# Optimization experiments

Hardware: AMD Instinct MI355X
Metric: run time of the kernel (lower is better)

The kernel has to match this reference:

```python
import jax, jax.numpy as jnp
import numpy as np

D_MODEL = 256
N_HEADS = 8
N_LEVELS = 3
N_POINTS = 4
HEAD_DIM = D_MODEL // N_HEADS
SPATIAL_SHAPES = [(80, 80), (40, 40), (20, 20)]
B = 16
LEN_Q = 300
N_TOTAL = sum(h * w for h, w in SPATIAL_SHAPES)  # 8400
N_LP = N_LEVELS * N_POINTS


def setup_inputs() -> dict:
    key = jax.random.key(0)
    ks = jax.random.split(key, 8)
    s = 0.02
    return {
        "query": jax.random.normal(ks[0], (B, LEN_Q, D_MODEL), jnp.float32),
        "reference_points": jax.random.uniform(ks[1], (B, LEN_Q, N_LEVELS, 2), jnp.float32),
        "input_flatten": jax.random.normal(ks[2], (B, N_TOTAL, D_MODEL), jnp.float32),
        "W_off": jax.random.normal(ks[3], (D_MODEL, N_HEADS * N_LP * 2), jnp.float32) * s,
        "b_off": jnp.zeros((N_HEADS * N_LP * 2,), jnp.float32),
        "W_attn": jax.random.normal(ks[4], (D_MODEL, N_HEADS * N_LP), jnp.float32) * s,
        "b_attn": jnp.zeros((N_HEADS * N_LP,), jnp.float32),
        "W_val": jax.random.normal(ks[5], (D_MODEL, D_MODEL), jnp.float32) * s,
        "b_val": jnp.zeros((D_MODEL,), jnp.float32),
        "W_out": jax.random.normal(ks[6], (D_MODEL, D_MODEL), jnp.float32) * s,
        "b_out": jnp.zeros((D_MODEL,), jnp.float32),
    }


def _ms_deform_core(value, sampling_locations, attention_weights):
    # value: (B, n_heads, head_dim, N_total); locations: (B, Lq, H, L, P, 2) in [0,1]
    Bq, Lq = sampling_locations.shape[0], sampling_locations.shape[1]
    BN = Bq * N_HEADS
    grids = 2.0 * sampling_locations - 1.0
    starts = np.cumsum([0] + [h * w for h, w in SPATIAL_SHAPES])
    sampled_levels = []
    for lid, (H, W) in enumerate(SPATIAL_SHAPES):
        val_l = value[..., starts[lid]:starts[lid + 1]]                    # (B,H,hd,HW)
        val_flat = val_l.reshape(BN, HEAD_DIM, H * W).transpose(0, 2, 1)   # (BN,HW,hd)
        g = grids[:, :, :, lid].transpose(0, 2, 1, 3, 4).reshape(BN, Lq, N_POINTS, 2)
        ix = ((g[..., 0] + 1.0) * W - 1.0) / 2.0
        iy = ((g[..., 1] + 1.0) * H - 1.0) / 2.0
        ix0 = jnp.floor(ix).astype(jnp.int32)
        iy0 = jnp.floor(iy).astype(jnp.int32)
        ix1 = ix0 + 1
        iy1 = iy0 + 1
        fx = (ix - ix0.astype(ix.dtype))[..., None]
        fy = (iy - iy0.astype(iy.dtype))[..., None]

        def corner(iyc, ixc):
            valid = ((ixc >= 0) & (ixc < W) & (iyc >= 0) & (iyc < H)).astype(val_flat.dtype)
            idx = (jnp.clip(iyc, 0, H - 1) * W + jnp.clip(ixc, 0, W - 1))
            idx = idx.reshape(BN, Lq * N_POINTS, 1)
            v = jnp.take_along_axis(val_flat, idx, axis=1)
            return v.reshape(BN, Lq, N_POINTS, HEAD_DIM) * valid[..., None]

        v00 = corner(iy0, ix0)
        v01 = corner(iy0, ix1)
        v10 = corner(iy1, ix0)
        v11 = corner(iy1, ix1)
        sampled = ((1 - fx) * (1 - fy)) * v00 + (fx * (1 - fy)) * v01 \
                + ((1 - fx) * fy) * v10 + (fx * fy) * v11
        sampled_levels.append(sampled.transpose(0, 3, 1, 2))               # (BN,hd,Lq,P)
    sv = jnp.stack(sampled_levels, axis=-2).reshape(BN, HEAD_DIM, Lq, N_LP)
    a = attention_weights.transpose(0, 2, 1, 3).reshape(BN, 1, Lq, N_LP)
    out = jnp.sum(sv * a, axis=-1)                                         # (BN,hd,Lq)
    return out.reshape(Bq, D_MODEL, Lq).transpose(0, 2, 1)                 # (B,Lq,D)


def reference(query, reference_points, input_flatten,
              W_off, b_off, W_attn, b_attn, W_val, b_val, W_out, b_out):
    Bq, Lq = query.shape[0], query.shape[1]
    value = input_flatten @ W_val + b_val
    value = value.reshape(Bq, -1, N_HEADS, HEAD_DIM).transpose(0, 2, 3, 1)  # (B,H,hd,N)
    off = (query @ W_off + b_off).reshape(Bq, Lq, N_HEADS, N_LEVELS, N_POINTS, 2)
    attn = jax.nn.softmax((query @ W_attn + b_attn).reshape(Bq, Lq, N_HEADS, N_LP), axis=-1)
    # offset normalizer is (W,H) per level (x first)
    norm = jnp.array([[w, h] for h, w in SPATIAL_SHAPES], jnp.float32)
    loc = reference_points[:, :, None, :, None, :] + off / norm[None, None, None, :, None, :]
    out = _ms_deform_core(value, loc, attn)
    return out @ W_out + b_out
```

## Files before the change

### kernel.cpp

```cpp
#include <hip/hip_runtime.h>
#include <hip/hip_bf16.h>

#define DM 256
#define NH 8
#define HD 32
#define NLV 3
#define NPT 4
#define NLP 12
#define BB 16
#define LQ 300
#define NT 8400
#define MROWS (BB * NT)
#define QROWS (BB * LQ)
#define KP 40

typedef __bf16 bf16x8 __attribute__((ext_vector_type(8)));
typedef float  f32x16 __attribute__((ext_vector_type(16)));

__global__ void k_wt(const float* __restrict__ W_val,
                     const float* __restrict__ W_off,
                     const float* __restrict__ W_attn,
                     __hip_bfloat16* __restrict__ Wt,
                     __hip_bfloat16* __restrict__ Wt2)
{
    const int n = blockIdx.x;
    const int k = threadIdx.x;
    if (n < 256) {
        Wt[(size_t)(k >> 5) * 8192 + n * 32 + (k & 31)] =
            __float2bfloat16(W_val[(size_t)k * 256 + n]);
    } else {
        const int n2 = n - 256;
        float v = (n2 < 192) ? W_off[(size_t)k * 192 + n2]
                             : W_attn[(size_t)k * 96 + (n2 - 192)];
        Wt2[(size_t)(k >> 5) * 9216 + n2 * 32 + (k & 31)] = __float2bfloat16(v);
    }
}

__global__ __launch_bounds__(256) void k_valproj(
    const float* __restrict__ A,
    const __hip_bfloat16* __restrict__ Wt,
    const float* __restrict__ bias,
    __hip_bfloat16* __restrict__ V)
{
    __shared__ __hip_bfloat16 As[64 * KP];
    __shared__ __hip_bfloat16 Ws[256 * KP];

    const int t    = threadIdx.x;
    const int m0   = blockIdx.x * 64;
    const int wave = t >> 6;
    const int lane = t & 63;
    const int lm   = lane & 31;
    const int lk   = (lane >> 5) * 8;

    f32x16 acc[2][2];
#pragma unroll
    for (int i = 0; i < 2; i++)
#pragma unroll
        for (int j = 0; j < 2; j++)
#pragma unroll
            for (int e = 0; e < 16; e++) acc[i][j][e] = 0.f;

    const int ar = t >> 2;
    const int ak = (t & 3) * 8;

    for (int kt = 0; kt < 256; kt += 32) {
        {
            const float* ap = A + (size_t)(m0 + ar) * 256 + kt + ak;
            float4 a0 = *(const float4*)ap;
            float4 a1 = *(const float4*)(ap + 4);
            union { __hip_bfloat162 h2[4]; bf16x8 v; } ua;
            ua.h2[0] = __float22bfloat162_rn(make_float2(a0.x, a0.y));
            ua.h2[1] = __float22bfloat162_rn(make_float2(a0.z, a0.w));
            ua.h2[2] = __float22bfloat162_rn(make_float2(a1.x, a1.y));
            ua.h2[3] = __float22bfloat162_rn(make_float2(a1.z, a1.w));
            *(bf16x8*)(As + ar * KP + ak) = ua.v;
        }
        {
            const __hip_bfloat16* wp = Wt + (size_t)(kt >> 5) * 8192 + t * 32;
            bf16x8 w0 = *(const bf16x8*)(wp + 0);
            bf16x8 w1 = *(const bf16x8*)(wp + 8);
            bf16x8 w2 = *(const bf16x8*)(wp + 16);
            bf16x8 w3 = *(const bf16x8*)(wp + 24);
            __hip_bfloat16* wd = Ws + t * KP;
            *(bf16x8*)(wd + 0)  = w0;
            *(bf16x8*)(wd + 8)  = w1;
            *(bf16x8*)(wd + 16) = w2;
            *(bf16x8*)(wd + 24) = w3;
        }
        __syncthreads();

#pragma unroll
        for (int kk = 0; kk < 32; kk += 16) {
            bf16x8 af0 = *(const bf16x8*)(As + (0 * 32 + lm) * KP + kk + lk);
            bf16x8 af1 = *(const bf16x8*)(As + (1 * 32 + lm) * KP + kk + lk);
            bf16x8 bf0 = *(const bf16x8*)(Ws + (wave * 64 + 0 * 32 + lm) * KP + kk + lk);
            bf16x8 bf1 = *(const bf16x8*)(Ws + (wave * 64 + 1 * 32 + lm) * KP + kk + lk);
            acc[0][0] = __builtin_amdgcn_mfma_f32_32x32x16_bf16(af0, bf0, acc[0][0], 0, 0, 0);
            acc[0][1] = __builtin_amdgcn_mfma_f32_32x32x16_bf16(af0, bf1, acc[0][1], 0, 0, 0);
            acc[1][0] = __builtin_amdgcn_mfma_f32_32x32x16_bf16(af1, bf0, acc[1][0], 0, 0, 0);
            acc[1][1] = __builtin_amdgcn_mfma_f32_32x32x16_bf16(af1, bf1, acc[1][1], 0, 0, 0);
        }
        __syncthreads();
    }

#pragma unroll
    for (int ni = 0; ni < 2; ni++) {
        const int n  = wave * 64 + ni * 32 + lm;
        const float bn = bias[n];
        const int h  = n >> 5;
        const int d  = n & 31;
#pragma unroll
        for (int mi = 0; mi < 2; mi++) {
#pragma unroll
            for (int r = 0; r < 16; r++) {
                int rl = (r & 3) + 8 * (r >> 2) + 4 * (lane >> 5);
                int m  = m0 + mi * 32 + rl;
                int b  = m / NT;
                int pos = m - b * NT;
                V[((size_t)(b * NH + h) * NT + pos) * HD + d] =
                    __float2bfloat16(acc[mi][ni][r] + bn);
            }
        }
    }
}

__global__ __launch_bounds__(192) void k_offattn(
    const float* __restrict__ Q,
    const __hip_bfloat16* __restrict__ Wt2,
    const float* __restrict__ boff,
    const float* __restrict__ battn,
    float* __restrict__ off_out,
    float* __restrict__ attn_out)
{
    __shared__ __hip_bfloat16 As[32 * KP];
    __shared__ __hip_bfloat16 Ws[288 * KP];

    const int t    = threadIdx.x;
    const int m0   = blockIdx.x * 32;
    const int wave = t >> 6;
    const int lane = t & 63;
    const int lm   = lane & 31;
    const int lk   = (lane >> 5) * 8;

    f32x16 acc[3];
#pragma unroll
    for (int j = 0; j < 3; j++)
#pragma unroll
        for (int e = 0; e < 16; e++) acc[j][e] = 0.f;

    for (int kt = 0; kt < 256; kt += 32) {
        if (t < 128) {
            const int ar = t >> 2;
            const int ak = (t & 3) * 8;
            const float* ap = Q + (size_t)(m0 + ar) * 256 + kt + ak;
            float4 a0 = *(const float4*)ap;
            float4 a1 = *(const float4*)(ap + 4);
            union { __hip_bfloat162 h2[4]; bf16x8 v; } ua;
            ua.h2[0] = __float22bfloat162_rn(make_float2(a0.x, a0.y));
            ua.h2[1] = __float22bfloat162_rn(make_float2(a0.z, a0.w));
            ua.h2[2] = __float22bfloat162_rn(make_float2(a1.x, a1.y));
            ua.h2[3] = __float22bfloat162_rn(make_float2(a1.z, a1.w));
            *(bf16x8*)(As + ar * KP + ak) = ua.v;
        }
        {
            const __hip_bfloat16* wp = Wt2 + (size_t)(kt >> 5) * 9216 + t * 32;
            __hip_bfloat16* wd = Ws + t * KP;
            *(bf16x8*)(wd + 0)  = *(const bf16x8*)(wp + 0);
            *(bf16x8*)(wd + 8)  = *(const bf16x8*)(wp + 8);
            *(bf16x8*)(wd + 16) = *(const bf16x8*)(wp + 16);
            *(bf16x8*)(wd + 24) = *(const bf16x8*)(wp + 24);
            if (t < 96) {
                const __hip_bfloat16* wp2 = Wt2 + (size_t)(kt >> 5) * 9216 + (t + 192) * 32;
                __hip_bfloat16* wd2 = Ws + (t + 192) * KP;
                *(bf16x8*)(wd2 + 0)  = *(const bf16x8*)(wp2 + 0);
                *(bf16x8*)(wd2 + 8)  = *(const bf16x8*)(wp2 + 8);
                *(bf16x8*)(wd2 + 16) = *(const bf16x8*)(wp2 + 16);
                *(bf16x8*)(wd2 + 24) = *(const bf16x8*)(wp2 + 24);
            }
        }
        __syncthreads();

#pragma unroll
        for (int kk = 0; kk < 32; kk += 16) {
            bf16x8 af = *(const bf16x8*)(As + lm * KP + kk + lk);
#pragma unroll
            for (int j = 0; j < 3; j++) {
                bf16x8 bf = *(const bf16x8*)(Ws + (wave * 96 + j * 32 + lm) * KP + kk + lk);
                acc[j] = __builtin_amdgcn_mfma_f32_32x32x16_bf16(af, bf, acc[j], 0, 0, 0);
            }
        }
        __syncthreads();
    }

#pragma unroll
    for (int j = 0; j < 3; j++) {
        const int n = wave * 96 + j * 32 + lm;
        const float bias_ = (n < 192) ? boff[n] : battn[n - 192];
#pragma unroll
        for (int r = 0; r < 16; r++) {
            int rl = (r & 3) + 8 * (r >> 2) + 4 * (lane >> 5);
            int m  = m0 + rl;
            float v = acc[j][r] + bias_;
            if (n < 192) off_out[(size_t)m * 192 + n] = v;
            else         attn_out[(size_t)m * 96 + (n - 192)] = v;
        }
    }
}

__global__ __launch_bounds__(256) void k_sample(
    const float* __restrict__ off_raw,
    const float* __restrict__ attn_raw,
    const float* __restrict__ refp,
    const __hip_bfloat16* __restrict__ V,
    float* __restrict__ sampled)
{
    const int t  = threadIdx.x;
    const int bq = blockIdx.x;
    const int b  = bq / LQ;

    __shared__ float aw[96];
    __shared__ float sx[96];
    __shared__ float sy[96];

    const float dims[3] = {80.f, 40.f, 20.f};

    if (t < 96) {
        int h = t / 12, lp = t - h * 12, l = lp >> 2, p = lp & 3;
        float ox = off_raw[(size_t)bq * 192 + ((h * 3 + l) * 4 + p) * 2 + 0];
        float oy = off_raw[(size_t)bq * 192 + ((h * 3 + l) * 4 + p) * 2 + 1];
        float rx = refp[(size_t)bq * 6 + l * 2 + 0];
        float ry = refp[(size_t)bq * 6 + l * 2 + 1];
        float D  = dims[l];
        float lx = rx + ox / D;
        float ly = ry + oy / D;
        sx[t] = lx * D - 0.5f;
        sy[t] = ly * D - 0.5f;
    }
    if (t < 8) {
        float v[12];
        float mx = -1e30f;
#pragma unroll
        for (int i = 0; i < 12; i++) {
            v[i] = attn_raw[(size_t)bq * 96 + t * 12 + i];
            mx = fmaxf(mx, v[i]);
        }
        float s = 0.f;
#pragma unroll
        for (int i = 0; i < 12; i++) { v[i] = expf(v[i] - mx); s += v[i]; }
        float inv = 1.f / s;
#pragma unroll
        for (int i = 0; i < 12; i++) aw[t * 12 + i] = v[i] * inv;
    }
    __syncthreads();

    const int h = t >> 5, d = t & 31;
    const __hip_bfloat16* vb = V + (size_t)(b * NH + h) * NT * HD + d;

    const int starts[3] = {0, 6400, 8000};
    const int idim[3]   = {80, 40, 20};

    float acc = 0.f;
#pragma unroll
    for (int l = 0; l < 3; l++) {
        const int Dl = idim[l];
        const int st = starts[l];
#pragma unroll
        for (int p = 0; p < 4; p++) {
            const int s = h * 12 + l * 4 + p;
            float ix = sx[s], iy = sy[s];
            float w  = aw[s];
            float fix = floorf(ix), fiy = floorf(iy);
            int ix0 = (int)fix, iy0 = (int)fiy;
            int ix1 = ix0 + 1, iy1 = iy0 + 1;
            float fx = ix - fix, fy = iy - fiy;

            float mx0 = (ix0 >= 0 && ix0 < Dl) ? 1.f : 0.f;
            float mx1 = (ix1 >= 0 && ix1 < Dl) ? 1.f : 0.f;
            float my0 = (iy0 >= 0 && iy0 < Dl) ? 1.f : 0.f;
            float my1 = (iy1 >= 0 && iy1 < Dl) ? 1.f : 0.f;

            int cx0 = min(max(ix0, 0), Dl - 1);
            int cx1 = min(max(ix1, 0), Dl - 1);
            int cy0 = min(max(iy0, 0), Dl - 1);
            int cy1 = min(max(iy1, 0), Dl - 1);

            float v00 = mx0 * my0 * __bfloat162float(vb[(size_t)(st + cy0 * Dl + cx0) * HD]);
            float v01 = mx1 * my0 * __bfloat162float(vb[(size_t)(st + cy0 * Dl + cx1) * HD]);
            float v10 = mx0 * my1 * __bfloat162float(vb[(size_t)(st + cy1 * Dl + cx0) * HD]);
            float v11 = mx1 * my1 * __bfloat162float(vb[(size_t)(st + cy1 * Dl + cx1) * HD]);

            float sval = (1.f - fx) * (1.f - fy) * v00 + fx * (1.f - fy) * v01
                       + (1.f - fx) * fy * v10 + fx * fy * v11;
            acc = fmaf(w, sval, acc);
        }
    }
    sampled[(size_t)bq * 256 + t] = acc;
}

__global__ __launch_bounds__(256) void k_outproj(
    const float* __restrict__ A,
    const float* __restrict__ W,
    const float* __restrict__ bias,
    float* __restrict__ out)
{
    __shared__ float As[32 * 33];
    __shared__ float Ws[32 * 256];
    const int t   = threadIdx.x;
    const int m0  = blockIdx.x * 32;
    const int tn  = (t & 31) * 8;
    const int tmg = (t >> 5) * 4;

    float acc[4][8];
#pragma unroll
    for (int i = 0; i < 4; i++)
#pragma unroll
        for (int j = 0; j < 8; j++) acc[i][j] = 0.f;

    for (int kt = 0; kt < 256; kt += 32) {
        {
            int f  = t;
            int r  = f >> 3;
            int kq = (f & 7) * 4;
            float4 a4 = *(const float4*)(A + (size_t)(m0 + r) * 256 + kt + kq);
            float* dst = &As[r * 33 + kq];
            dst[0] = a4.x; dst[1] = a4.y; dst[2] = a4.z; dst[3] = a4.w;
        }
#pragma unroll
        for (int i = 0; i < 8; i++) {
            int f  = t + i * 256;
            int kr = f >> 6;
            int cq = (f & 63) * 4;
            *(float4*)(&Ws[kr * 256 + cq]) =
                *(const float4*)(W + (size_t)(kt + kr) * 256 + cq);
        }
        __syncthreads();
#pragma unroll 4
        for (int k = 0; k < 32; k++) {
            float a[4], w[8];
#pragma unroll
            for (int i = 0; i < 4; i++) a[i] = As[(tmg + i) * 33 + k];
            float4 w0 = *(float4*)(&Ws[k * 256 + tn]);
            float4 w1 = *(float4*)(&Ws[k * 256 + tn + 4]);
            w[0] = w0.x; w[1] = w0.y; w[2] = w0.z; w[3] = w0.w;
            w[4] = w1.x; w[5] = w1.y; w[6] = w1.z; w[7] = w1.w;
#pragma unroll
            for (int i = 0; i < 4; i++)
#pragma unroll
                for (int j = 0; j < 8; j++)
                    acc[i][j] = fmaf(a[i], w[j], acc[i][j]);
        }
        __syncthreads();
    }

    float bv[8];
#pragma unroll
    for (int j = 0; j < 8; j++) bv[j] = bias[tn + j];
#pragma unroll
    for (int i = 0; i < 4; i++) {
        int m = m0 + tmg + i;
        float4 o0, o1;
        o0.x = acc[i][0] + bv[0]; o0.y = acc[i][1] + bv[1];
        o0.z = acc[i][2] + bv[2]; o0.w = acc[i][3] + bv[3];
        o1.x = acc[i][4] + bv[4]; o1.y = acc[i][5] + bv[5];
        o1.z = acc[i][6] + bv[6]; o1.w = acc[i][7] + bv[7];
        *(float4*)(out + (size_t)m * 256 + tn)     = o0;
        *(float4*)(out + (size_t)m * 256 + tn + 4) = o1;
    }
}

extern "C" void kernel_launch(void* const* d_in, const int* in_sizes, int n_in,
                              void* d_out, int out_size, void* d_ws, size_t ws_size,
                              hipStream_t stream) {
    const float* query  = (const float*)d_in[0];
    const float* refp   = (const float*)d_in[1];
    const float* inputf = (const float*)d_in[2];
    const float* W_off  = (const float*)d_in[3];
    const float* b_off  = (const float*)d_in[4];
    const float* W_attn = (const float*)d_in[5];
    const float* b_attn = (const float*)d_in[6];
    const float* W_val  = (const float*)d_in[7];
    const float* b_val  = (const float*)d_in[8];
    const float* W_out  = (const float*)d_in[9];
    const float* b_out  = (const float*)d_in[10];
    float* out = (float*)d_out;

    char* ws = (char*)d_ws;
    const size_t value_bytes = (size_t)BB * NH * NT * HD * 2;
    const size_t off_bytes   = (size_t)QROWS * 192 * 4;
    const size_t attn_bytes  = (size_t)QROWS * 96 * 4;
    __hip_bfloat16* value = (__hip_bfloat16*)ws;
    float* off_raw  = (float*)(ws + value_bytes);
    float* attn_raw = (float*)(ws + value_bytes + off_bytes);
    float* sampled  = (float*)(ws + value_bytes + off_bytes + attn_bytes);
    __hip_bfloat16* Wt  = (__hip_bfloat16*)sampled;
    __hip_bfloat16* Wt2 = (__hip_bfloat16*)((char*)sampled + 131072);

    k_wt<<<544, 256, 0, stream>>>(W_val, W_off, W_attn, Wt, Wt2);
    k_valproj<<<MROWS / 64, 256, 0, stream>>>(inputf, Wt, b_val, value);
    k_offattn<<<QROWS / 32, 192, 0, stream>>>(query, Wt2, b_off, b_attn,
                                              off_raw, attn_raw);
    k_sample<<<QROWS, 256, 0, stream>>>(off_raw, attn_raw, refp, value, sampled);
    k_outproj<<<QROWS / 32, 256, 0, stream>>>(sampled, W_out, b_out, out);
}
```

Before: 326.6 us.

## Double-buffer value projection, vectorize sampling, and move output projection to bf16 MFMA

The value projection GEMM gains double-buffered LDS tiles, with next-tile global loads issued before the MFMAs, so one barrier per k-step is removed and load latency is hidden. The sampling kernel now handles two queries per block and precomputes corner weights and indices in shared memory. Each thread gathers two channels with bf16x2 loads and writes bf16 output. The output projection switches from an fp32 FMA GEMM to bf16 MFMA using a pre-transposed bf16 W_out, which adds rounding error on the sampled activations.

New measurement: 283.4 us. 1.15x faster.

```diff
diff --git a/kernel.cpp b/kernel.cpp
--- a/kernel.cpp
+++ b/kernel.cpp
@@ -15,24 +15,31 @@
 #define KP 40
 
 typedef __bf16 bf16x8 __attribute__((ext_vector_type(8)));
+typedef __bf16 bf16x4 __attribute__((ext_vector_type(4)));
 typedef float  f32x16 __attribute__((ext_vector_type(16)));
 
 __global__ void k_wt(const float* __restrict__ W_val,
                      const float* __restrict__ W_off,
                      const float* __restrict__ W_attn,
+                     const float* __restrict__ W_out,
                      __hip_bfloat16* __restrict__ Wt,
-                     __hip_bfloat16* __restrict__ Wt2)
+                     __hip_bfloat16* __restrict__ Wt2,
+                     __hip_bfloat16* __restrict__ Wt3)
 {
     const int n = blockIdx.x;
     const int k = threadIdx.x;
     if (n < 256) {
         Wt[(size_t)(k >> 5) * 8192 + n * 32 + (k & 31)] =
             __float2bfloat16(W_val[(size_t)k * 256 + n]);
-    } else {
+    } else if (n < 544) {
         const int n2 = n - 256;
         float v = (n2 < 192) ? W_off[(size_t)k * 192 + n2]
                              : W_attn[(size_t)k * 96 + (n2 - 192)];
         Wt2[(size_t)(k >> 5) * 9216 + n2 * 32 + (k & 31)] = __float2bfloat16(v);
+    } else {
+        const int n3 = n - 544;
+        Wt3[(size_t)(k >> 5) * 8192 + n3 * 32 + (k & 31)] =
+            __float2bfloat16(W_out[(size_t)k * 256 + n3]);
     }
 }
 
@@ -42,8 +49,8 @@
     const float* __restrict__ bias,
     __hip_bfloat16* __restrict__ V)
 {
-    __shared__ __hip_bfloat16 As[64 * KP];
-    __shared__ __hip_bfloat16 Ws[256 * KP];
+    __shared__ __hip_bfloat16 As[2][64 * KP];
+    __shared__ __hip_bfloat16 Ws[2][256 * KP];
 
     const int t    = threadIdx.x;
     const int m0   = blockIdx.x * 64;
@@ -63,44 +70,75 @@
     const int ar = t >> 2;
     const int ak = (t & 3) * 8;
 
-    for (int kt = 0; kt < 256; kt += 32) {
-        {
+    float4 a0, a1;
+    bf16x8 w0, w1, w2, w3;
+
+    {
+        const float* ap = A + (size_t)(m0 + ar) * 256 + ak;
+        a0 = *(const float4*)ap;
+        a1 = *(const float4*)(ap + 4);
+        const __hip_bfloat16* wp = Wt + t * 32;
+        w0 = *(const bf16x8*)(wp + 0);
+        w1 = *(const bf16x8*)(wp + 8);
+        w2 = *(const bf16x8*)(wp + 16);
+        w3 = *(const bf16x8*)(wp + 24);
+    }
+    {
+        union { __hip_bfloat162 h2[4]; bf16x8 v; } ua;
+        ua.h2[0] = __float22bfloat162_rn(make_float2(a0.x, a0.y));
+        ua.h2[1] = __float22bfloat162_rn(make_float2(a0.z, a0.w));
+        ua.h2[2] = __float22bfloat162_rn(make_float2(a1.x, a1.y));
+        ua.h2[3] = __float22bfloat162_rn(make_float2(a1.z, a1.w));
+        *(bf16x8*)(&As[0][ar * KP + ak]) = ua.v;
+        __hip_bfloat16* wd = &Ws[0][t * KP];
+        *(bf16x8*)(wd + 0)  = w0;
+        *(bf16x8*)(wd + 8)  = w1;
+        *(bf16x8*)(wd + 16) = w2;
+        *(bf16x8*)(wd + 24) = w3;
+    }
+    __syncthreads();
+
+    for (int it = 0; it < 8; ++it) {
+        float4 na0, na1;
+        bf16x8 nw0, nw1, nw2, nw3;
+        if (it < 7) {
+            const int kt = (it + 1) * 32;
             const float* ap = A + (size_t)(m0 + ar) * 256 + kt + ak;
-            float4 a0 = *(const float4*)ap;
-            float4 a1 = *(const float4*)(ap + 4);
-            union { __hip_bfloat162 h2[4]; bf16x8 v; } ua;
-            ua.h2[0] = __float22bfloat162_rn(make_float2(a0.x, a0.y));
-            ua.h2[1] = __float22bfloat162_rn(make_float2(a0.z, a0.w));
-            ua.h2[2] = __float22bfloat162_rn(make_float2(a1.x, a1.y));
-            ua.h2[3] = __float22bfloat162_rn(make_float2(a1.z, a1.w));
-            *(bf16x8*)(As + ar * KP + ak) = ua.v;
-        }
-        {
-            const __hip_bfloat16* wp = Wt + (size_t)(kt >> 5) * 8192 + t * 32;
-            bf16x8 w0 = *(const bf16x8*)(wp + 0);
-            bf16x8 w1 = *(const bf16x8*)(wp + 8);
-            bf16x8 w2 = *(const bf16x8*)(wp + 16);
-            bf16x8 w3 = *(const bf16x8*)(wp + 24);
-            __hip_bfloat16* wd = Ws + t * KP;
-            *(bf16x8*)(wd + 0)  = w0;
-            *(bf16x8*)(wd + 8)  = w1;
-            *(bf16x8*)(wd + 16) = w2;
-            *(bf16x8*)(wd + 24) = w3;
-        }
-        __syncthreads();
-
+            na0 = *(const float4*)ap;
+            na1 = *(const float4*)(ap + 4);
+            const __hip_bfloat16* wp = Wt + (size_t)(it + 1) * 8192 + t * 32;
+            nw0 = *(const bf16x8*)(wp + 0);
+            nw1 = *(const bf16x8*)(wp + 8);
+            nw2 = *(const bf16x8*)(wp + 16);
+            nw3 = *(const bf16x8*)(wp + 24);
+        }
+        const int buf = it & 1;
 #pragma unroll
         for (int kk = 0; kk < 32; kk += 16) {
-            bf16x8 af0 = *(const bf16x8*)(As + (0 * 32 + lm) * KP + kk + lk);
-            bf16x8 af1 = *(const bf16x8*)(As + (1 * 32 + lm) * KP + kk + lk);
-            bf16x8 bf0 = *(const bf16x8*)(Ws + (wave * 64 + 0 * 32 + lm) * KP + kk + lk);
-            bf16x8 bf1 = *(const bf16x8*)(Ws + (wave * 64 + 1 * 32 + lm) * KP + kk + lk);
+            bf16x8 af0 = *(const bf16x8*)(&As[buf][(0 * 32 + lm) * KP + kk + lk]);
+            bf16x8 af1 = *(const bf16x8*)(&As[buf][(1 * 32 + lm) * KP + kk + lk]);
+            bf16x8 bf0 = *(const bf16x8*)(&Ws[buf][(wave * 64 + 0 * 32 + lm) * KP + kk + lk]);
+            bf16x8 bf1 = *(const bf16x8*)(&Ws[buf][(wave * 64 + 1 * 32 + lm) * KP + kk + lk]);
             acc[0][0] = __builtin_amdgcn_mfma_f32_32x32x16_bf16(af0, bf0, acc[0][0], 0, 0, 0);
             acc[0][1] = __builtin_amdgcn_mfma_f32_32x32x16_bf16(af0, bf1, acc[0][1], 0, 0, 0);
             acc[1][0] = __builtin_amdgcn_mfma_f32_32x32x16_bf16(af1, bf0, acc[1][0], 0, 0, 0);
             acc[1][1] = __builtin_amdgcn_mfma_f32_32x32x16_bf16(af1, bf1, acc[1][1], 0, 0, 0);
         }
-        __syncthreads();
+        if (it < 7) {
+            union { __hip_bfloat162 h2[4]; bf16x8 v; } ua;
+            ua.h2[0] = __float22bfloat162_rn(make_float2(na0.x, na0.y));
+            ua.h2[1] = __float22bfloat162_rn(make_float2(na0.z, na0.w));
+            ua.h2[2] = __float22bfloat162_rn(make_float2(na1.x, na1.y));
+            ua.h2[3] = __float22bfloat162_rn(make_float2(na1.z, na1.w));
+            const int nb = buf ^ 1;
+            *(bf16x8*)(&As[nb][ar * KP + ak]) = ua.v;
+            __hip_bfloat16* wd = &Ws[nb][t * KP];
+            *(bf16x8*)(wd + 0)  = nw0;
+            *(bf16x8*)(wd + 8)  = nw1;
+            *(bf16x8*)(wd + 16) = nw2;
+            *(bf16x8*)(wd + 24) = nw3;
+            __syncthreads();
+        }
     }
 
 #pragma unroll
@@ -212,20 +250,40 @@
     const float* __restrict__ attn_raw,
     const float* __restrict__ refp,
     const __hip_bfloat16* __restrict__ V,
-    float* __restrict__ sampled)
+    __hip_bfloat16* __restrict__ sampled)
 {
     const int t  = threadIdx.x;
-    const int bq = blockIdx.x;
+    const int q2 = t >> 7;
+    const int tq = t & 127;
+    const int bq = blockIdx.x * 2 + q2;
     const int b  = bq / LQ;
 
-    __shared__ float aw[96];
-    __shared__ float sx[96];
-    __shared__ float sy[96];
-
-    const float dims[3] = {80.f, 40.f, 20.f};
-
-    if (t < 96) {
-        int h = t / 12, lp = t - h * 12, l = lp >> 2, p = lp & 3;
+    __shared__ float aw[2][96];
+    __shared__ float wc[2][96][4];
+    __shared__ int   ic[2][96][4];
+
+    if (tq < 8) {
+        float v[12];
+        float mx = -1e30f;
+#pragma unroll
+        for (int i = 0; i < 12; i++) {
+            v[i] = attn_raw[(size_t)bq * 96 + tq * 12 + i];
+            mx = fmaxf(mx, v[i]);
+        }
+        float s = 0.f;
+#pragma unroll
+        for (int i = 0; i < 12; i++) { v[i] = expf(v[i] - mx); s += v[i]; }
+        float inv = 1.f / s;
+#pragma unroll
+        for (int i = 0; i < 12; i++) aw[q2][tq * 12 + i] = v[i] * inv;
+    }
+    __syncthreads();
+
+    if (tq < 96) {
+        const float dims[3]  = {80.f, 40.f, 20.f};
+        const int startsl[3] = {0, 6400, 8000};
+        const int idiml[3]   = {80, 40, 20};
+        int h = tq / 12, lp = tq - h * 12, l = lp >> 2, p = lp & 3;
         float ox = off_raw[(size_t)bq * 192 + ((h * 3 + l) * 4 + p) * 2 + 0];
         float oy = off_raw[(size_t)bq * 192 + ((h * 3 + l) * 4 + p) * 2 + 1];
         float rx = refp[(size_t)bq * 6 + l * 2 + 0];
@@ -233,138 +291,118 @@
         float D  = dims[l];
         float lx = rx + ox / D;
         float ly = ry + oy / D;
-        sx[t] = lx * D - 0.5f;
-        sy[t] = ly * D - 0.5f;
-    }
-    if (t < 8) {
-        float v[12];
-        float mx = -1e30f;
-#pragma unroll
-        for (int i = 0; i < 12; i++) {
-            v[i] = attn_raw[(size_t)bq * 96 + t * 12 + i];
-            mx = fmaxf(mx, v[i]);
-        }
-        float s = 0.f;
-#pragma unroll
-        for (int i = 0; i < 12; i++) { v[i] = expf(v[i] - mx); s += v[i]; }
-        float inv = 1.f / s;
-#pragma unroll
-        for (int i = 0; i < 12; i++) aw[t * 12 + i] = v[i] * inv;
+        float ix = lx * D - 0.5f;
+        float iy = ly * D - 0.5f;
+        const int Dl = idiml[l];
+        const int st = startsl[l];
+
+        float fix = floorf(ix), fiy = floorf(iy);
+        int ix0 = (int)fix, iy0 = (int)fiy;
+        int ix1 = ix0 + 1, iy1 = iy0 + 1;
+        float fx = ix - fix, fy = iy - fiy;
+
+        float mx0 = (ix0 >= 0 && ix0 < Dl) ? 1.f : 0.f;
+        float mx1 = (ix1 >= 0 && ix1 < Dl) ? 1.f : 0.f;
+        float my0 = (iy0 >= 0 && iy0 < Dl) ? 1.f : 0.f;
+        float my1 = (iy1 >= 0 && iy1 < Dl) ? 1.f : 0.f;
+
+        int cx0 = min(max(ix0, 0), Dl - 1);
+        int cx1 = min(max(ix1, 0), Dl - 1);
+        int cy0 = min(max(iy0, 0), Dl - 1);
+        int cy1 = min(max(iy1, 0), Dl - 1);
+
+        float a = aw[q2][tq];
+        wc[q2][tq][0] = (1.f - fx) * (1.f - fy) * mx0 * my0 * a;
+        wc[q2][tq][1] = fx * (1.f - fy) * mx1 * my0 * a;
+        wc[q2][tq][2] = (1.f - fx) * fy * mx0 * my1 * a;
+        wc[q2][tq][3] = fx * fy * mx1 * my1 * a;
+        ic[q2][tq][0] = (st + cy0 * Dl + cx0) * HD;
+        ic[q2][tq][1] = (st + cy0 * Dl + cx1) * HD;
+        ic[q2][tq][2] = (st + cy1 * Dl + cx0) * HD;
+        ic[q2][tq][3] = (st + cy1 * Dl + cx1) * HD;
     }
     __syncthreads();
 
-    const int h = t >> 5, d = t & 31;
-    const __hip_bfloat16* vb = V + (size_t)(b * NH + h) * NT * HD + d;
-
-    const int starts[3] = {0, 6400, 8000};
-    const int idim[3]   = {80, 40, 20};
-
-    float acc = 0.f;
-#pragma unroll
-    for (int l = 0; l < 3; l++) {
-        const int Dl = idim[l];
-        const int st = starts[l];
-#pragma unroll
-        for (int p = 0; p < 4; p++) {
-            const int s = h * 12 + l * 4 + p;
-            float ix = sx[s], iy = sy[s];
-            float w  = aw[s];
-            float fix = floorf(ix), fiy = floorf(iy);
-            int ix0 = (int)fix, iy0 = (int)fiy;
-            int ix1 = ix0 + 1, iy1 = iy0 + 1;
-            float fx = ix - fix, fy = iy - fiy;
-
-            float mx0 = (ix0 >= 0 && ix0 < Dl) ? 1.f : 0.f;
-            float mx1 = (ix1 >= 0 && ix1 < Dl) ? 1.f : 0.f;
-            float my0 = (iy0 >= 0 && iy0 < Dl) ? 1.f : 0.f;
-            float my1 = (iy1 >= 0 && iy1 < Dl) ? 1.f : 0.f;
-
-            int cx0 = min(max(ix0, 0), Dl - 1);
-            int cx1 = min(max(ix1, 0), Dl - 1);
-            int cy0 = min(max(iy0, 0), Dl - 1);
-            int cy1 = min(max(iy1, 0), Dl - 1);
-
-            float v00 = mx0 * my0 * __bfloat162float(vb[(size_t)(st + cy0 * Dl + cx0) * HD]);
-            float v01 = mx1 * my0 * __bfloat162float(vb[(size_t)(st + cy0 * Dl + cx1) * HD]);
-            float v10 = mx0 * my1 * __bfloat162float(vb[(size_t)(st + cy1 * Dl + cx0) * HD]);
-            float v11 = mx1 * my1 * __bfloat162float(vb[(size_t)(st + cy1 * Dl + cx1) * HD]);
-
-            float sval = (1.f - fx) * (1.f - fy) * v00 + fx * (1.f - fy) * v01
-                       + (1.f - fx) * fy * v10 + fx * fy * v11;
-            acc = fmaf(w, sval, acc);
-        }
-    }
-    sampled[(size_t)bq * 256 + t] = acc;
+    const int h  = tq >> 4;
+    const int dp = (tq & 15) * 2;
+    const __hip_bfloat16* vb = V + (size_t)(b * NH + h) * NT * HD + dp;
+
+    float acc0 = 0.f, acc1 = 0.f;
+#pragma unroll
+    for (int lp = 0; lp < 12; lp++) {
+        const int s = h * 12 + lp;
+        float4 w4 = *(const float4*)(&wc[q2][s][0]);
+        int4   i4 = *(const int4*)(&ic[q2][s][0]);
+        float2 v00 = __bfloat1622float2(*(const __hip_bfloat162*)(vb + i4.x));
+        float2 v01 = __bfloat1622float2(*(const __hip_bfloat162*)(vb + i4.y));
+        float2 v10 = __bfloat1622float2(*(const __hip_bfloat162*)(vb + i4.z));
+        float2 v11 = __bfloat1622float2(*(const __hip_bfloat162*)(vb + i4.w));
+        acc0 = fmaf(w4.x, v00.x, fmaf(w4.y, v01.x, fmaf(w4.z, v10.x, fmaf(w4.w, v11.x, acc0))));
+        acc1 = fmaf(w4.x, v00.y, fmaf(w4.y, v01.y, fmaf(w4.z, v10.y, fmaf(w4.w, v11.y, acc1))));
+    }
+    *(__hip_bfloat162*)(sampled + (size_t)bq * 256 + h * 32 + dp) =
+        __float22bfloat162_rn(make_float2(acc0, acc1));
 }
 
 __global__ __launch_bounds__(256) void k_outproj(
-    const float* __restrict__ A,
-    const float* __restrict__ W,
+    const __hip_bfloat16* __restrict__ A,
+    const __hip_bfloat16* __restrict__ Wt3,
     const float* __restrict__ bias,
     float* __restrict__ out)
 {
-    __shared__ float As[32 * 33];
-    __shared__ float Ws[32 * 256];
-    const int t   = threadIdx.x;
-    const int m0  = blockIdx.x * 32;
-    const int tn  = (t & 31) * 8;
-    const int tmg = (t >> 5) * 4;
-
-    float acc[4][8];
-#pragma unroll
-    for (int i = 0; i < 4; i++)
-#pragma unroll
-        for (int j = 0; j < 8; j++) acc[i][j] = 0.f;
+    __shared__ __hip_bfloat16 As[32 * KP];
+    __shared__ __hip_bfloat16 Ws[256 * KP];
+
+    const int t    = threadIdx.x;
+    const int m0   = blockIdx.x * 32;
+    const int wave = t >> 6;
+    const int lane = t & 63;
+    const int lm   = lane & 31;
+    const int lk   = (lane >> 5) * 8;
+
+    f32x16 acc[2];
+#pragma unroll
+    for (int j = 0; j < 2; j++)
+#pragma unroll
+        for (int e = 0; e < 16; e++) acc[j][e] = 0.f;
+
+    const int ar = t >> 3;
+    const int ak = (t & 7) * 4;
 
     for (int kt = 0; kt < 256; kt += 32) {
+        *(bf16x4*)(As + ar * KP + ak) =
+            *(const bf16x4*)(A + (size_t)(m0 + ar) * 256 + kt + ak);
         {
-            int f  = t;
-            int r  = f >> 3;
-            int kq = (f & 7) * 4;
-            float4 a4 = *(const float4*)(A + (size_t)(m0 + r) * 256 + kt + kq);
-            float* dst = &As[r * 33 + kq];
-            dst[0] = a4.x; dst[1] = a4.y; dst[2] = a4.z; dst[3] = a4.w;
-        }
-#pragma unroll
-        for (int i = 0; i < 8; i++) {
-            int f  = t + i * 256;
-            int kr = f >> 6;
-            int cq = (f & 63) * 4;
-            *(float4*)(&Ws[kr * 256 + cq]) =
-                *(const float4*)(W + (size_t)(kt + kr) * 256 + cq);
+            const __hip_bfloat16* wp = Wt3 + (size_t)(kt >> 5) * 8192 + t * 32;
+            __hip_bfloat16* wd = Ws + t * KP;
+            *(bf16x8*)(wd + 0)  = *(const bf16x8*)(wp + 0);
+            *(bf16x8*)(wd + 8)  = *(const bf16x8*)(wp + 8);
+            *(bf16x8*)(wd + 16) = *(const bf16x8*)(wp + 16);
+            *(bf16x8*)(wd + 24) = *(const bf16x8*)(wp + 24);
         }
         __syncthreads();
-#pragma unroll 4
-        for (int k = 0; k < 32; k++) {
-            float a[4], w[8];
-#pragma unroll
-            for (int i = 0; i < 4; i++) a[i] = As[(tmg + i) * 33 + k];
-            float4 w0 = *(float4*)(&Ws[k * 256 + tn]);
-            float4 w1 = *(float4*)(&Ws[k * 256 + tn + 4]);
-            w[0] = w0.x; w[1] = w0.y; w[2] = w0.z; w[3] = w0.w;
-            w[4] = w1.x; w[5] = w1.y; w[6] = w1.z; w[7] = w1.w;
-#pragma unroll
-            for (int i = 0; i < 4; i++)
-#pragma unroll
-                for (int j = 0; j < 8; j++)
-                    acc[i][j] = fmaf(a[i], w[j], acc[i][j]);
+
+#pragma unroll
+        for (int kk = 0; kk < 32; kk += 16) {
+            bf16x8 af = *(const bf16x8*)(As + lm * KP + kk + lk);
+            bf16x8 bf0 = *(const bf16x8*)(Ws + (wave * 64 + 0 * 32 + lm) * KP + kk + lk);
+            bf16x8 bf1 = *(const bf16x8*)(Ws + (wave * 64 + 1 * 32 + lm) * KP + kk + lk);
+            acc[0] = __builtin_amdgcn_mfma_f32_32x32x16_bf16(af, bf0, acc[0], 0, 0, 0);
+            acc[1] = __builtin_amdgcn_mfma_f32_32x32x16_bf16(af, bf1, acc[1], 0, 0, 0);
         }
         __syncthreads();
     }
 
-    float bv[8];
-#pragma unroll
-    for (int j = 0; j < 8; j++) bv[j] = bias[tn + j];
-#pragma unroll
-    for (int i = 0; i < 4; i++) {
-        int m = m0 + tmg + i;
-        float4 o0, o1;
-        o0.x = acc[i][0] + bv[0]; o0.y = acc[i][1] + bv[1];
-        o0.z = acc[i][2] + bv[2]; o0.w = acc[i][3] + bv[3];
-        o1.x = acc[i][4] + bv[4]; o1.y = acc[i][5] + bv[5];
-        o1.z = acc[i][6] + bv[6]; o1.w = acc[i][7] + bv[7];
-        *(float4*)(out + (size_t)m * 256 + tn)     = o0;
-        *(float4*)(out + (size_t)m * 256 + tn + 4) = o1;
+#pragma unroll
+    for (int j = 0; j < 2; j++) {
+        const int n = wave * 64 + j * 32 + lm;
+        const float bn = bias[n];
+#pragma unroll
+        for (int r = 0; r < 16; r++) {
+            int rl = (r & 3) + 8 * (r >> 2) + 4 * (lane >> 5);
+            int m  = m0 + rl;
+            out[(size_t)m * 256 + n] = acc[j][r] + bn;
+        }
     }
 }
 
@@ -385,20 +423,18 @@
     float* out = (float*)d_out;
 
     char* ws = (char*)d_ws;
-    const size_t value_bytes = (size_t)BB * NH * NT * HD * 2;
-    const size_t off_bytes   = (size_t)QROWS * 192 * 4;
-    const size_t attn_bytes  = (size_t)QROWS * 96 * 4;
-    __hip_bfloat16* value = (__hip_bfloat16*)ws;
-    float* off_raw  = (float*)(ws + value_bytes);
-    float* attn_raw = (float*)(ws + value_bytes + off_bytes);
-    float* sampled  = (float*)(ws + value_bytes + off_bytes + attn_bytes);
-    __hip_bfloat16* Wt  = (__hip_bfloat16*)sampled;
-    __hip_bfloat16* Wt2 = (__hip_bfloat16*)((char*)sampled + 131072);
-
-    k_wt<<<544, 256, 0, stream>>>(W_val, W_off, W_attn, Wt, Wt2);
+    __hip_bfloat16* value   = (__hip_bfloat16*)ws;
+    float* off_raw          = (float*)(ws + 68812800);
+    float* attn_raw         = (float*)(ws + 72499200);
+    __hip_bfloat16* sampled = (__hip_bfloat16*)(ws + 74342400);
+    __hip_bfloat16* Wt      = (__hip_bfloat16*)(ws + 76800000);
+    __hip_bfloat16* Wt2     = (__hip_bfloat16*)(ws + 76931072);
+    __hip_bfloat16* Wt3     = (__hip_bfloat16*)(ws + 77078528);
+
+    k_wt<<<800, 256, 0, stream>>>(W_val, W_off, W_attn, W_out, Wt, Wt2, Wt3);
     k_valproj<<<MROWS / 64, 256, 0, stream>>>(inputf, Wt, b_val, value);
     k_offattn<<<QROWS / 32, 192, 0, stream>>>(query, Wt2, b_off, b_attn,
                                               off_raw, attn_raw);
-    k_sample<<<QROWS, 256, 0, stream>>>(off_raw, attn_raw, refp, value, sampled);
-    k_outproj<<<QROWS / 32, 256, 0, stream>>>(sampled, W_out, b_out, out);
-}
+    k_sample<<<QROWS / 2, 256, 0, stream>>>(off_raw, attn_raw, refp, value, sampled);
+    k_outproj<<<QROWS / 32, 256, 0, stream>>>(sampled, Wt3, b_out, out);
+}
```
